# Kernel optimization log

Measured on AMD Instinct MI355X. Metric: run time of the kernel, lower is better.

## Reference

```python
import jax, jax.numpy as jnp
import numpy as np

DIM = 320; D_STATE = 32; D_CONV = 4; HEADDIM = 80; D_INNER = 640; NHEADS = 8
CONV_DIM = D_INNER + 2 * D_STATE          # 704
D_IN_PROJ = 2 * D_INNER + 2 * D_STATE + NHEADS  # 1352
ATTN_HEADS = 4; MLP_DIM = 1024; DEPTH = 2; INNER = DIM // 2  # cross-attn downsample_rate=2
PATCH = (128.0, 256.0, 256.0); IMG = (16, 32, 32); NPTS = 6; BATCH = 2
EPS = 1e-5
TWO_PI = 2.0 * np.pi


def layernorm(x, w, b):
    m = x.mean(-1, keepdims=True)
    v = ((x - m) ** 2).mean(-1, keepdims=True)
    return (x - m) * jax.lax.rsqrt(v + EPS) * w + b


def pe_encode(coords, gauss):
    # coords in [0,1], last dim 3 -> random fourier features (sin|cos) of width DIM
    c = TWO_PI * ((2.0 * coords - 1.0) @ gauss)
    return jnp.concatenate([jnp.sin(c), jnp.cos(c)], -1)


def mha(qi, ki, vi, wq, bq, wk, bk, wv, bv, wo, bo):
    q = qi @ wq.T + bq
    k = ki @ wk.T + bk
    v = vi @ wv.T + bv
    B, Nq, Ci = q.shape
    hd = Ci // ATTN_HEADS
    q = q.reshape(B, Nq, ATTN_HEADS, hd)
    k = k.reshape(B, -1, ATTN_HEADS, hd)
    v = v.reshape(B, -1, ATTN_HEADS, hd)
    att = jax.nn.softmax(jnp.einsum('bqhd,bkhd->bhqk', q, k) / np.sqrt(hd), -1)
    o = jnp.einsum('bhqk,bkhd->bqhd', att, v).reshape(B, Nq, Ci)
    return o @ wo.T + bo


def mamba2(xn, in_w, conv_w, conv_b, dt_bias, A_log, Dp, rms_w, out_w):
    Bt, L, _ = xn.shape
    zxbcdt = xn @ in_w.T                                    # (B,L,1352)
    z, xBC, dt = jnp.split(zxbcdt, [D_INNER, D_INNER + CONV_DIM], axis=-1)
    dt = jax.nn.softplus(dt + dt_bias)                      # (B,L,H)
    # causal depthwise conv over sequence, kernel D_CONV
    pad = jnp.pad(xBC, ((0, 0), (D_CONV - 1, 0), (0, 0)))
    conv = conv_b + sum(pad[:, k:k + L] * conv_w[:, k] for k in range(D_CONV))
    xBC = jax.nn.silu(conv)
    xs, Bm, Cm = jnp.split(xBC, [D_INNER, D_INNER + D_STATE], axis=-1)
    A = -jnp.exp(A_log)                                     # (H,)
    xh = xs.reshape(Bt, L, NHEADS, HEADDIM)

    def step(S, inp):  # S: (B,H,N,P)
        dt_t, x_t, B_t, C_t = inp  # (B,H),(B,H,P),(B,N),(B,N)
        decay = jnp.exp(dt_t * A)
        S = S * decay[..., None, None] + (dt_t[..., None, None] * B_t[:, None, :, None]) * x_t[:, :, None, :]
        y = jnp.einsum('bn,bhnp->bhp', C_t, S)
        return S, y

    S0 = jnp.zeros((Bt, NHEADS, D_STATE, HEADDIM), xn.dtype)
    _, ys = jax.lax.scan(step, S0, (dt.transpose(1, 0, 2), xh.transpose(1, 0, 2, 3), Bm.transpose(1, 0, 2), Cm.transpose(1, 0, 2)))
    y = ys.transpose(1, 0, 2, 3) + Dp[None, None, :, None] * xh  # (B,L,H,P)
    y = y.reshape(Bt, L, D_INNER)
    y = y * jax.nn.silu(z)                                  # gated RMSNorm (norm_before_gate=False)
    y = y * jax.lax.rsqrt((y * y).mean(-1, keepdims=True) + EPS) * rms_w
    return y @ out_w.T


def _forward(x, coords, ln_w, ln_b, in_w, conv_w, conv_b, dt_bias, A_log, Dp, rms_w, out_w,
             pe_gauss, point_tab, sa_w, sa_b, t2i_w, t2i_b, t2i_ow, t2i_ob,
             i2t_w, i2t_b, i2t_ow, i2t_ob, norms_w, norms_b, mlp_w1, mlp_b1, mlp_w2, mlp_b2, labels):
    B, C = x.shape[:2]
    img = x.shape[2:]
    n = int(np.prod(img))
    xf = jnp.transpose(x.reshape(B, C, n), (0, 2, 1))       # (B,n,C)
    keys = mamba2(layernorm(xf, ln_w, ln_b), in_w, conv_w, conv_b, dt_bias, A_log, Dp, rms_w, out_w)
    # point embeddings: fourier PE of normalized click coords + label embedding
    point_emb = pe_encode(coords / jnp.asarray(PATCH, x.dtype), pe_gauss) + point_tab[labels]
    # dense image positional encoding over the feature grid
    axes = [(jnp.arange(s, dtype=x.dtype) + 0.5) / s for s in img]
    grid = jnp.stack(jnp.meshgrid(*axes, indexing='ij'), -1)  # (d,h,w,3)
    kpe = jnp.broadcast_to(pe_encode(grid, pe_gauss).reshape(1, n, C), (B, n, C))
    queries = point_emb
    qpe = point_emb
    for i in range(DEPTH):
        saw, sab = sa_w[i], sa_b[i]
        if i == 0:  # skip_first_layer_pe
            queries = mha(queries, queries, queries, saw[0], sab[0], saw[1], sab[1], saw[2], sab[2], saw[3], sab[3])
        else:
            q = queries + qpe
            queries = queries + mha(q, q, queries, saw[0], sab[0], saw[1], sab[1], saw[2], sab[2], saw[3], sab[3])
        queries = layernorm(queries, norms_w[i, 0], norms_b[i, 0])
        q = queries + qpe
        k = keys + kpe
        queries = queries + mha(q, k, keys, t2i_w[i, 0], t2i_b[i, 0], t2i_w[i, 1], t2i_b[i, 1], t2i_w[i, 2], t2i_b[i, 2], t2i_ow[i], t2i_ob[i])
        queries = layernorm(queries, norms_w[i, 1], norms_b[i, 1])
        queries = queries + jax.nn.relu(queries @ mlp_w1[i].T + mlp_b1[i]) @ mlp_w2[i].T + mlp_b2[i]
        queries = layernorm(queries, norms_w[i, 2], norms_b[i, 2])
        q = queries + qpe
        k = keys + kpe
        keys = keys + mha(k, q, queries, i2t_w[i, 0], i2t_b[i, 0], i2t_w[i, 1], i2t_b[i, 1], i2t_w[i, 2], i2t_b[i, 2], i2t_ow[i], i2t_ob[i])
        keys = layernorm(keys, norms_w[i, 3], norms_b[i, 3])
    return jnp.transpose(keys, (0, 2, 1)).reshape(B, C, *img)


def setup_inputs():
    key = jax.random.key(0)
    ks = iter(jax.random.split(key, 64))
    f32 = jnp.float32

    def nrm(shape, s=0.02):
        return s * jax.random.normal(next(ks), shape, dtype=f32)

    inp = {}
    inp['x'] = jax.random.normal(next(ks), (BATCH, DIM) + IMG, dtype=f32)
    inp['coords'] = jax.random.uniform(next(ks), (BATCH, NPTS, 3), dtype=f32) * jnp.asarray(PATCH, f32)
    inp['labels'] = jax.random.randint(next(ks), (BATCH, NPTS), 0, 2)
    inp['ln_w'] = jnp.ones((DIM,), f32)
    inp['ln_b'] = jnp.zeros((DIM,), f32)
    inp['in_w'] = nrm((D_IN_PROJ, DIM))
    inp['conv_w'] = nrm((CONV_DIM, D_CONV), 0.2)
    inp['conv_b'] = jnp.zeros((CONV_DIM,), f32)
    inp['dt_bias'] = nrm((NHEADS,), 0.1)
    inp['A_log'] = jnp.log(jnp.arange(1, NHEADS + 1, dtype=f32))
    inp['Dp'] = jnp.ones((NHEADS,), f32)
    inp['rms_w'] = jnp.ones((D_INNER,), f32)
    inp['out_w'] = nrm((DIM, D_INNER))
    inp['pe_gauss'] = jax.random.normal(next(ks), (3, DIM // 2), dtype=f32)
    inp['point_tab'] = nrm((2, DIM), 1.0)
    inp['sa_w'] = nrm((DEPTH, 4, DIM, DIM))
    inp['sa_b'] = jnp.zeros((DEPTH, 4, DIM), f32)
    inp['t2i_w'] = nrm((DEPTH, 3, INNER, DIM))
    inp['t2i_b'] = jnp.zeros((DEPTH, 3, INNER), f32)
    inp['t2i_ow'] = nrm((DEPTH, DIM, INNER))
    inp['t2i_ob'] = jnp.zeros((DEPTH, DIM), f32)
    inp['i2t_w'] = nrm((DEPTH, 3, INNER, DIM))
    inp['i2t_b'] = jnp.zeros((DEPTH, 3, INNER), f32)
    inp['i2t_ow'] = nrm((DEPTH, DIM, INNER))
    inp['i2t_ob'] = jnp.zeros((DEPTH, DIM), f32)
    inp['norms_w'] = jnp.ones((DEPTH, 4, DIM), f32)
    inp['norms_b'] = jnp.zeros((DEPTH, 4, DIM), f32)
    inp['mlp_w1'] = nrm((DEPTH, MLP_DIM, DIM))
    inp['mlp_b1'] = jnp.zeros((DEPTH, MLP_DIM), f32)
    inp['mlp_w2'] = nrm((DEPTH, DIM, MLP_DIM))
    inp['mlp_b2'] = jnp.zeros((DEPTH, DIM), f32)
    return inp


def reference(x, coords, labels, ln_w, ln_b, in_w, conv_w, conv_b, dt_bias, A_log, Dp, rms_w, out_w,
              pe_gauss, point_tab, sa_w, sa_b, t2i_w, t2i_b, t2i_ow, t2i_ob,
              i2t_w, i2t_b, i2t_ow, i2t_ob, norms_w, norms_b, mlp_w1, mlp_b1, mlp_w2, mlp_b2):
    return _forward(x, coords, ln_w, ln_b, in_w, conv_w, conv_b, dt_bias, A_log, Dp, rms_w, out_w,
                    pe_gauss, point_tab, sa_w, sa_b, t2i_w, t2i_b, t2i_ow, t2i_ob,
                    i2t_w, i2t_b, i2t_ow, i2t_ob, norms_w, norms_b, mlp_w1, mlp_b1, mlp_w2, mlp_b2, labels)
```

## Files before the change

### kernel.cpp

```cpp
#include <hip/hip_runtime.h>
#include <math.h>

#define LSEQ 16384
#define CDIM 320
#define DIN 640
#define NHH 8
#define CONVD 704
#define XBCW 712
#define YSTR 704
#define QCH 64
#define NCHUNK 256

typedef __bf16 bf16_t;
typedef __bf16 bf16x8 __attribute__((ext_vector_type(8)));
typedef __bf16 bf16x4 __attribute__((ext_vector_type(4)));
typedef float f32x4 __attribute__((ext_vector_type(4)));

__device__ __forceinline__ float wave_sum(float v) {
#pragma unroll
  for (int o = 32; o > 0; o >>= 1) v += __shfl_down(v, o, 64);
  return v;
}
__device__ __forceinline__ float wave_max(float v) {
#pragma unroll
  for (int o = 32; o > 0; o >>= 1) v = fmaxf(v, __shfl_down(v, o, 64));
  return v;
}
__device__ __forceinline__ float block_sum256(float v, float* red) {
  int tid = threadIdx.x;
  v = wave_sum(v);
  __syncthreads();
  if ((tid & 63) == 0) red[tid >> 6] = v;
// ... 93 lines not shown
  float* xp = io + (size_t)row * CDIM;
  int lane = threadIdx.x & 63;
  float x[5];
  float s = 0.f;
#pragma unroll
  for (int k = 0; k < 5; ++k) { x[k] = xp[lane + 64 * k]; s += x[k]; }
  s = wave_sum(s); s = __shfl(s, 0, 64);
  float mean = s * (1.f / 320.f);
  float v = 0.f;
#pragma unroll
  for (int k = 0; k < 5; ++k) { float t = x[k] - mean; v += t * t; }
  v = wave_sum(v); v = __shfl(v, 0, 64);
  float rstd = rsqrtf(v * (1.f / 320.f) + 1e-5f);
#pragma unroll
  for (int k = 0; k < 5; ++k) {
    int i = lane + 64 * k;
    xp[i] = (x[k] - mean) * rstd * w[i] + b[i];
  }
}

__global__ __launch_bounds__(256) void gemm_bf(
    const void* __restrict__ A, const void* __restrict__ W,
    const float* __restrict__ bias, const float* __restrict__ pe,
    float* __restrict__ C, float* __restrict__ C2,
    const void* __restrict__ W2, const float* __restrict__ bias2, int wsplit,
    int M, int N, int K, int lda, int ldc, int nsplit, int ldc2,
    int addC, int abf, int wbf, long long sA, long long sC) {
  int z = blockIdx.z;
  C += (size_t)z * sC;
  if (C2) C2 += (size_t)z * sC;
  int gx = gridDim.x;
  int nwg = gx * gridDim.y;
  int lin = blockIdx.y * gx + blockIdx.x;
  int xcd = lin & 7, idx = lin >> 3;
  int q = nwg >> 3, r = nwg & 7;
  int base = (xcd < r) ? xcd * (q + 1) : r * (q + 1) + (xcd - r) * q;
  int lin2 = base + idx;
  int mblk = lin2 / gx, nblk = lin2 % gx;
  int m0 = mblk << 7, n0 = nblk << 6;

  __shared__ __align__(16) bf16_t As[2][4096];
  __shared__ __align__(16) bf16_t Ws[2][2048];
  int tid = threadIdx.x;
  int wave = tid >> 6, lane = tid & 63;
  int fm = lane & 15, quad = lane >> 4;
  int rA = tid >> 1, hA = tid & 1;
  int rW = tid >> 2, qW = tid & 3;
  const float* ag = nullptr;
  const bf16_t* agb = nullptr;
  const float* peg = nullptr;
  if (abf) {
    agb = (const bf16_t*)A + (size_t)z * sA + (size_t)(m0 + rA) * lda + hA * 16;
  } else {
// ... 89 lines not shown
    bf16x8 b3 = *(bf16x8*)&Ws[buf][1536 + lane * 8];
    acc[0][0] = __builtin_amdgcn_mfma_f32_16x16x32_bf16(af0, b0, acc[0][0], 0, 0, 0);
    acc[0][1] = __builtin_amdgcn_mfma_f32_16x16x32_bf16(af0, b1, acc[0][1], 0, 0, 0);
    acc[0][2] = __builtin_amdgcn_mfma_f32_16x16x32_bf16(af0, b2, acc[0][2], 0, 0, 0);
    acc[0][3] = __builtin_amdgcn_mfma_f32_16x16x32_bf16(af0, b3, acc[0][3], 0, 0, 0);
    acc[1][0] = __builtin_amdgcn_mfma_f32_16x16x32_bf16(af1, b0, acc[1][0], 0, 0, 0);
    acc[1][1] = __builtin_amdgcn_mfma_f32_16x16x32_bf16(af1, b1, acc[1][1], 0, 0, 0);
    acc[1][2] = __builtin_amdgcn_mfma_f32_16x16x32_bf16(af1, b2, acc[1][2], 0, 0, 0);
    acc[1][3] = __builtin_amdgcn_mfma_f32_16x16x32_bf16(af1, b3, acc[1][3], 0, 0, 0);
    if (more) {
      packLDS(buf ^ 1);
      __syncthreads();
    }
  }
#pragma unroll
  for (int ms = 0; ms < 2; ++ms)
#pragma unroll
    for (int ns = 0; ns < 4; ++ns) {
      int n = n0 + ns * 16 + fm;
      if (n >= N) continue;
      float bv = 0.f;
      if (n < wsplit) { if (bias) bv = bias[n]; }
      else            { if (bias2) bv = bias2[n - wsplit]; }
      float* Cb;
      int ldcb, nc;
      if (n < nsplit) { Cb = C; ldcb = ldc; nc = n; }
      else           { Cb = C2; ldcb = ldc2; nc = n - nsplit; }
#pragma unroll
      for (int rr = 0; rr < 4; ++rr) {
        int m = m0 + wave * 32 + ms * 16 + quad * 4 + rr;
        float v = acc[ms][ns][rr] + bv;
        size_t off = (size_t)m * ldcb + nc;
        if (addC) v += Cb[off];
        Cb[off] = v;
      }
    }
}

__global__ __launch_bounds__(256) void smallmm(
    const float* __restrict__ A, const float* __restrict__ A2,
    const float* __restrict__ W, const float* __restrict__ bias,
    float* __restrict__ C, int N, int K, int addC, int relu, int a2lim) {
  int wave = threadIdx.x >> 6, lane = threadIdx.x & 63;
  int n = blockIdx.x * 4 + wave;
  if (n >= N) return;
  const float* w = W + (size_t)n * K;
  bool useA2 = (A2 != nullptr) && (n < a2lim);
  float part[12];
#pragma unroll
  for (int m = 0; m < 12; ++m) part[m] = 0.f;
  for (int k0 = 0; k0 < K; k0 += 64) {
    int k = k0 + lane;
    if (k < K) {
      float wv = w[k];
      const float* ap = A + k;
      if (useA2) {
        const float* ap2 = A2 + k;
// ... 1 lines not shown
        for (int m = 0; m < 12; ++m)
          part[m] = fmaf(ap[(size_t)m * K] + ap2[(size_t)m * K], wv, part[m]);
      } else {
#pragma unroll
        for (int m = 0; m < 12; ++m)
          part[m] = fmaf(ap[(size_t)m * K], wv, part[m]);
      }
    }
  }
  float bv = bias ? bias[n] : 0.f;
#pragma unroll
  for (int m = 0; m < 12; ++m) {
    float dot = wave_sum(part[m]);
    if (lane == 0) {
      float v = dot + bv;
      if (relu) v = fmaxf(v, 0.f);
      size_t off = (size_t)m * N + n;
      if (addC) v += C[off];
      C[off] = v;
    }
  }
}

__global__ void dt_kernel(const float* __restrict__ XBC, const float* __restrict__ dt_bias,
                          float* __restrict__ dtbuf) {
  int idx = blockIdx.x * 256 + threadIdx.x;
  if (idx >= LSEQ * NHH) return;
  int h = idx & 7;
  int t = idx >> 3;
  float v = XBC[(size_t)t * XBCW + 704 + h] + dt_bias[h];
  float sp = (v > 20.f) ? v : log1pf(expf(v));
  dtbuf[(size_t)h * LSEQ + t] = sp;
}

__global__ __launch_bounds__(256) void conv2(const float* __restrict__ XBC,
                                             const float* __restrict__ conv_w,
                                             const float* __restrict__ conv_b,
                                             float* __restrict__ Cv) {
  int lane = threadIdx.x & 63, wv = threadIdx.x >> 6;
  int d = blockIdx.x * 64 + lane;
  int t0 = (blockIdx.y * 4 + wv) * 32;
  float w0 = conv_w[d * 4 + 0], w1 = conv_w[d * 4 + 1];
  float w2 = conv_w[d * 4 + 2], w3 = conv_w[d * 4 + 3];
  float bv = conv_b[d];
  const float* src = XBC + d;
  float xm3, xm2, xm1;
  if (t0 == 0) {
    xm3 = 0.f; xm2 = 0.f; xm1 = 0.f;
  } else {
    xm3 = src[(size_t)(t0 - 3) * XBCW];
    xm2 = src[(size_t)(t0 - 2) * XBCW];
    xm1 = src[(size_t)(t0 - 1) * XBCW];
  }
#pragma unroll 8
  for (int t = t0; t < t0 + 32; ++t) {
    float xt = src[(size_t)t * XBCW];
    float a = bv + xm3 * w0 + xm2 * w1 + xm1 * w2 + xt * w3;
    Cv[(size_t)t * CONVD + d] = a / (1.f + expf(-a));
    xm3 = xm2; xm2 = xm1; xm1 = xt;
  }
}

__global__ __launch_bounds__(256) void scan_a(const float* __restrict__ Cv,
                                              const float* __restrict__ dtbuf,
                                              const float* __restrict__ A_log,
                                              float* __restrict__ Schunk,
                                              float* __restrict__ cabuf) {
  int c = blockIdx.x, h = blockIdx.y;
  int t0 = c * QCH;
  __shared__ float sdt[64], sca[64], sw[64];
  __shared__ __align__(16) float sB[64][36];
  __shared__ __align__(16) float sXt[80][68];
  int tid = threadIdx.x;
  float Aval = -expf(A_log[h]);
  if (tid < 64) sdt[tid] = dtbuf[(size_t)h * LSEQ + t0 + tid];
  __syncthreads();
  if (tid == 0) {
    float run = 0.f;
    for (int j = 0; j < 64; ++j) { run += sdt[j] * Aval; sca[j] = run; }
  }
  __syncthreads();
  float caend = sca[63];
  if (tid < 64) {
    sw[tid] = expf(caend - sca[tid]) * sdt[tid];
    cabuf[(size_t)h * LSEQ + t0 + tid] = sca[tid];
  }
  for (int i = tid; i < 2048; i += 256) {
    int j = i >> 5, n = i & 31;
    sB[j][n] = Cv[(size_t)(t0 + j) * CONVD + 640 + n];
  }
  for (int i = tid; i < 5120; i += 256) {
    int j = i / 80, p = i % 80;
    sXt[p][j] = Cv[(size_t)(t0 + j) * CONVD + h * 80 + p];
  }
  __syncthreads();
  int n = tid >> 3, pb = tid & 7;
  float acc[10];
#pragma unroll
  for (int u = 0; u < 10; ++u) acc[u] = 0.f;
  for (int jb = 0; jb < 16; ++jb) {
    float wB[4];
#pragma unroll
    for (int jj = 0; jj < 4; ++jj) {
      int j = jb * 4 + jj;
      wB[jj] = sw[j] * sB[j][n];
    }
#pragma unroll
    for (int u = 0; u < 10; ++u) {
      int p = pb * 10 + u;
      float4 x4 = *(const float4*)&sXt[p][jb * 4];
      acc[u] += wB[0] * x4.x + wB[1] * x4.y + wB[2] * x4.z + wB[3] * x4.w;
    }
  }
  float* outp = Schunk + (size_t)(h * NCHUNK + c) * 2560;
#pragma unroll
  for (int u = 0; u < 10; ++u) outp[n * 80 + pb * 10 + u] = acc[u];
}

__global__ __launch_bounds__(256) void scan_b(const float* __restrict__ Schunk,
                                              const float* __restrict__ cabuf,
                                              float* __restrict__ Sprev) {
  int pc = blockIdx.x, h = blockIdx.y;
  __shared__ float sdec[256];
  int tid = threadIdx.x;
  sdec[tid] = expf(cabuf[(size_t)h * LSEQ + tid * 64 + 63]);
  __syncthreads();
  int e = pc * 256 + tid;
  const float* base = Schunk + (size_t)h * NCHUNK * 2560 + e;
  float* pbase = Sprev + (size_t)h * NCHUNK * 2560 + e;
  float s = 0.f;
  float v = base[0];
  for (int c = 0; c < NCHUNK; ++c) {
    float vn = (c < NCHUNK - 1) ? base[(size_t)(c + 1) * 2560] : 0.f;
    pbase[(size_t)c * 2560] = s;
    s = s * sdec[c] + v;
    v = vn;
  }
}

__global__ __launch_bounds__(256) void scan_c(const float* __restrict__ Cv,
                                              const float* __restrict__ dtbuf,
                                              const float* __restrict__ cabuf,
                                              const float* __restrict__ Sprev,
                                              const float* __restrict__ Dp,
                                              float* __restrict__ Y) {
  int c = blockIdx.x, h = blockIdx.y;
  int t0 = c * QCH;
  __shared__ float sdt[64], sca[64], sexp[64];
  __shared__ __align__(16) bf16_t sC[64 * 40];
  __shared__ __align__(16) bf16_t sB[64 * 40];
  __shared__ __align__(16) bf16_t sXt[80 * 72];
  __shared__ __align__(16) bf16_t sSt[80 * 40];
  __shared__ __align__(16) bf16_t sP[64 * 72];
  int tid = threadIdx.x;
  int wave = tid >> 6, lane = tid & 63;
  int fm = lane & 15, quad = lane >> 4;
  if (tid < 64) {
    sdt[tid] = dtbuf[(size_t)h * LSEQ + t0 + tid];
    float cav = cabuf[(size_t)h * LSEQ + t0 + tid];
    sca[tid] = cav;
    sexp[tid] = expf(cav);
  }
  for (int i = tid; i < 2048; i += 256) {
    int j = i >> 5, n = i & 31;
    size_t base = (size_t)(t0 + j) * CONVD;
    sB[j * 40 + n] = (bf16_t)Cv[base + 640 + n];
    sC[j * 40 + n] = (bf16_t)Cv[base + 672 + n];
  }
  for (int i = tid; i < 5120; i += 256) {
    int j = i / 80, p = i % 80;
    sXt[p * 72 + j] = (bf16_t)Cv[(size_t)(t0 + j) * CONVD + h * 80 + p];
  }
  {
    const float* sp = Sprev + (size_t)(h * NCHUNK + c) * 2560;
    for (int i = tid; i < 2560; i += 256) {
      int n = i / 80, p = i % 80;
      sSt[p * 40 + n] = (bf16_t)sp[i];
    }
  }
  __syncthreads();
  int m0 = wave * 16;
  int jbase = m0 + quad * 4;
  bf16x8 afC = *(bf16x8*)&sC[(m0 + fm) * 40 + quad * 8];
  f32x4 accS[4];
#pragma unroll
  for (int nt = 0; nt < 4; ++nt) {
    bf16x8 bf = *(bf16x8*)&sB[(nt * 16 + fm) * 40 + quad * 8];
    f32x4 zero = (f32x4){0.f, 0.f, 0.f, 0.f};
    accS[nt] = __builtin_amdgcn_mfma_f32_16x16x32_bf16(afC, bf, zero, 0, 0, 0);
  }
  float scaj[4];
#pragma unroll
  for (int r = 0; r < 4; ++r) scaj[r] = sca[jbase + r];
#pragma unroll
// ... 19 lines not shown
#pragma unroll
  for (int r = 0; r < 4; ++r) gj[r] = sexp[jbase + r];
#pragma unroll
  for (int pt = 0; pt < 5; ++pt)
#pragma unroll
    for (int r = 0; r < 4; ++r) acc[pt][r] *= gj[r];
  bf16x8 afP0 = *(bf16x8*)&sP[(m0 + fm) * 72 + 0 + quad * 8];
  bf16x8 afP1 = *(bf16x8*)&sP[(m0 + fm) * 72 + 32 + quad * 8];
#pragma unroll
  for (int pt = 0; pt < 5; ++pt) {
    bf16x8 bx0 = *(bf16x8*)&sXt[(pt * 16 + fm) * 72 + 0 + quad * 8];
    bf16x8 bx1 = *(bf16x8*)&sXt[(pt * 16 + fm) * 72 + 32 + quad * 8];
    acc[pt] = __builtin_amdgcn_mfma_f32_16x16x32_bf16(afP0, bx0, acc[pt], 0, 0, 0);
    acc[pt] = __builtin_amdgcn_mfma_f32_16x16x32_bf16(afP1, bx1, acc[pt], 0, 0, 0);
  }
  float dval = Dp[h];
#pragma unroll
  for (int pt = 0; pt < 5; ++pt) {
    int p = pt * 16 + fm;
#pragma unroll
    for (int r = 0; r < 4; ++r) {
      int j = jbase + r;
      float xv = (float)sXt[p * 72 + j];
      Y[(size_t)(t0 + j) * YSTR + h * 80 + p] = acc[pt][r] + dval * xv;
    }
  }
}

__global__ __launch_bounds__(256) void gate_rms(const float* __restrict__ Y,
                                                const float* __restrict__ Z,
                                                const float* __restrict__ rms_w,
                                                bf16_t* __restrict__ YB) {
  __shared__ float red[4];
  size_t row = blockIdx.x;
  const float* y = Y + row * YSTR;
  const float* z = Z + row * DIN;
  bf16_t* yo = YB + row * DIN;
  int tid = threadIdx.x;
  float g0, g1, g2 = 0.f;
  {
    float zi = z[tid];
    g0 = y[tid] * (zi / (1.f + expf(-zi)));
    zi = z[tid + 256];
    g1 = y[tid + 256] * (zi / (1.f + expf(-zi)));
    if (tid + 512 < DIN) {
      zi = z[tid + 512];
      g2 = y[tid + 512] * (zi / (1.f + expf(-zi)));
    }
  }
  float ss = g0 * g0 + g1 * g1 + g2 * g2;
  float tot = block_sum256(ss, red);
  float r = rsqrtf(tot / (float)DIN + 1e-5f);
  yo[tid] = (bf16_t)(g0 * r * rms_w[tid]);
  yo[tid + 256] = (bf16_t)(g1 * r * rms_w[tid + 256]);
  if (tid + 512 < DIN) yo[tid + 512] = (bf16_t)(g2 * r * rms_w[tid + 512]);
}

__global__ void kpe_kernel(const float* __restrict__ gauss, float* __restrict__ KPE) {
  int idx = blockIdx.x * 256 + threadIdx.x;
  if (idx >= LSEQ * 160) return;
  int f = idx % 160, t = idx / 160;
  int d = t >> 10, hh = (t >> 5) & 31, w = t & 31;
  float vx = 2.f * ((d + 0.5f) / 16.f) - 1.f;
  float vy = 2.f * ((hh + 0.5f) / 32.f) - 1.f;
  float vz = 2.f * ((w + 0.5f) / 32.f) - 1.f;
  float cc = 6.28318530717958647692f * (vx * gauss[f] + vy * gauss[160 + f] + vz * gauss[320 + f]);
  KPE[(size_t)t * CDIM + f] = sinf(cc);
  KPE[(size_t)t * CDIM + 160 + f] = cosf(cc);
}

__global__ void point_kernel(const float* __restrict__ coords, const int* __restrict__ labels,
                             const float* __restrict__ gauss, const float* __restrict__ ptab,
                             float* __restrict__ qpe, float* __restrict__ queries) {
  int idx = blockIdx.x * 64 + threadIdx.x;
  if (idx >= 12 * 160) return;
  int f = idx % 160, pt = idx / 160;
  const float* co = coords + pt * 3;
  float vx = 2.f * (co[0] / 128.f) - 1.f;
// ... 22 lines not shown
    float d = 0.f;
    for (int p = 0; p < 80; ++p) d += sq[qi][p] * sk[ki][p];
    sw[qi][ki] = d * 0.11180339887498948f;
  }
  __syncthreads();
  if (tid < 6) {
    float mx = sw[tid][0];
    for (int k = 1; k < 6; ++k) mx = fmaxf(mx, sw[tid][k]);
    float s = 0.f;
    for (int k = 0; k < 6; ++k) { float e = expf(sw[tid][k] - mx); sw[tid][k] = e; s += e; }
    float inv = 1.f / s;
    for (int k = 0; k < 6; ++k) sw[tid][k] *= inv;
  }
  __syncthreads();
  for (int i = tid; i < 480; i += 128) {
    int qi = i / 80, p = i % 80;
    float o = 0.f;
    for (int k = 0; k < 6; ++k) o += sw[qi][k] * sv[k][p];
    O[(size_t)(b * 6 + qi) * CDIM + h * 80 + p] = o;
  }
}

__global__ __launch_bounds__(256) void attn_t2i_part2(const float* __restrict__ Qp,
                                                      const float* __restrict__ Kp,
                                                      const float* __restrict__ Vp,
                                                      float* __restrict__ Part) {
  int b = blockIdx.z, h = blockIdx.y, c = blockIdx.x;
  Qp += (size_t)b * 960;
  Kp += (size_t)b * LSEQ * 160;
  Vp += (size_t)b * LSEQ * 160;
  Part += (size_t)b * 24 * 64 * 42;
  __shared__ float sq[240];
  __shared__ float redm[4][6], reds[4][6];
  __shared__ __align__(16) bf16_t sPb[16 * 264];
  __shared__ __align__(16) bf16_t sVtb[48 * 264];
  int tid = threadIdx.x;
  int wave = tid >> 6, lane = tid & 63;
  if (tid < 240) sq[tid] = Qp[(size_t)(tid / 40) * 160 + h * 40 + (tid % 40)];
  __syncthreads();
  int t = c * 256 + tid;
  const float* kp = Kp + (size_t)t * 160 + h * 40;
  float kr[40];
#pragma unroll
  for (int v = 0; v < 10; ++v) {
    float4 k4 = *(const float4*)(kp + v * 4);
    kr[v * 4 + 0] = k4.x; kr[v * 4 + 1] = k4.y; kr[v * 4 + 2] = k4.z; kr[v * 4 + 3] = k4.w;
  }
  const float* vp = Vp + (size_t)t * 160 + h * 40;
#pragma unroll
  for (int v = 0; v < 10; ++v) {
    float4 v4 = *(const float4*)(vp + v * 4);
    sVtb[(v * 4 + 0) * 264 + tid] = (bf16_t)v4.x;
    sVtb[(v * 4 + 1) * 264 + tid] = (bf16_t)v4.y;
    sVtb[(v * 4 + 2) * 264 + tid] = (bf16_t)v4.z;
    sVtb[(v * 4 + 3) * 264 + tid] = (bf16_t)v4.w;
  }
  float s[6];
#pragma unroll
  for (int qi = 0; qi < 6; ++qi) {
    float d = 0.f;
#pragma unroll
    for (int p = 0; p < 40; ++p) d += sq[qi * 40 + p] * kr[p];
    s[qi] = d * 0.15811388300841897f;
  }
#pragma unroll
  for (int qi = 0; qi < 6; ++qi) {
    float wm = wave_max(s[qi]);
    if (lane == 0) redm[wave][qi] = wm;
  }
  __syncthreads();
  float gmax[6], ls[6];
#pragma unroll
  for (int qi = 0; qi < 6; ++qi)
    gmax[qi] = fmaxf(fmaxf(redm[0][qi], redm[1][qi]), fmaxf(redm[2][qi], redm[3][qi]));
#pragma unroll
  for (int qi = 0; qi < 6; ++qi) {
    float e = expf(s[qi] - gmax[qi]);
    sPb[qi * 264 + tid] = (bf16_t)e;
// ... 47 lines not shown
  const float* base = Part + (size_t)b * 24 * 64 * 42 + (size_t)blk * 64 * 42;
  float m = base[j * 42 + 40], l = base[j * 42 + 41];
  float gmax = wave_max(m);
  gmax = __shfl(gmax, 0, 64);
  float sc = expf(m - gmax);
  float tot = wave_sum(l * sc);
  tot = __shfl(tot, 0, 64);
  float inv = 1.f / tot;
  __shared__ float ssc[64];
  ssc[j] = sc;
  __syncthreads();
  if (j < 40) {
    float a0 = 0.f, a1 = 0.f, a2 = 0.f, a3 = 0.f;
    for (int jj = 0; jj < 64; jj += 4) {
      a0 = fmaf(base[(jj + 0) * 42 + j], ssc[jj + 0], a0);
      a1 = fmaf(base[(jj + 1) * 42 + j], ssc[jj + 1], a1);
      a2 = fmaf(base[(jj + 2) * 42 + j], ssc[jj + 2], a2);
      a3 = fmaf(base[(jj + 3) * 42 + j], ssc[jj + 3], a3);
    }
    O[(size_t)b * 960 + (size_t)qi * 160 + h * 40 + j] = (a0 + a1 + a2 + a3) * inv;
  }
}

__global__ __launch_bounds__(256) void attn_i2t(const float* __restrict__ Qp,
                                                const float* __restrict__ KV,
                                                bf16_t* __restrict__ O) {
  int h = blockIdx.y, b = blockIdx.z;
  int t = blockIdx.x * 256 + threadIdx.x;
  Qp += (size_t)b * LSEQ * 160;
  O += (size_t)b * LSEQ * 160;
  __shared__ float sk[6][40], sv[6][40];
  if (threadIdx.x < 240) {
    int tok = threadIdx.x / 40, p = threadIdx.x % 40;
    const float* base = KV + (size_t)(b * 6 + tok) * 320 + h * 40 + p;
    sk[tok][p] = base[0];
    sv[tok][p] = base[160];
  }
  __syncthreads();
  const float* q = Qp + (size_t)t * 160 + h * 40;
  float qr[40];
#pragma unroll
  for (int v = 0; v < 10; ++v) {
    float4 q4 = *(const float4*)(q + v * 4);
    qr[v * 4 + 0] = q4.x; qr[v * 4 + 1] = q4.y; qr[v * 4 + 2] = q4.z; qr[v * 4 + 3] = q4.w;
  }
  float s[6];
#pragma unroll
  for (int k = 0; k < 6; ++k) {
    float d = 0.f;
    for (int p = 0; p < 40; ++p) d += qr[p] * sk[k][p];
    s[k] = d * 0.15811388300841897f;
  }
  float mx = s[0];
#pragma unroll
  for (int k = 1; k < 6; ++k) mx = fmaxf(mx, s[k]);
  float sum = 0.f;
#pragma unroll
  for (int k = 0; k < 6; ++k) { s[k] = expf(s[k] - mx); sum += s[k]; }
  float inv = 1.f / sum;
  bf16_t* o = O + (size_t)t * 160 + h * 40;
#pragma unroll
  for (int v = 0; v < 10; ++v) {
    float o0 = 0.f, o1 = 0.f, o2 = 0.f, o3 = 0.f;
#pragma unroll
    for (int k = 0; k < 6; ++k) {
      float w = s[k];
      o0 += w * sv[k][v * 4 + 0];
// ... 36 lines not shown
  const float* i2t_w   = (const float*)d_in[21];
  const float* i2t_b   = (const float*)d_in[22];
  const float* i2t_ow  = (const float*)d_in[23];
  const float* i2t_ob  = (const float*)d_in[24];
  const float* norms_w = (const float*)d_in[25];
  const float* norms_b = (const float*)d_in[26];
  const float* mlp_w1  = (const float*)d_in[27];
  const float* mlp_b1  = (const float*)d_in[28];
  const float* mlp_w2  = (const float*)d_in[29];
  const float* mlp_b2  = (const float*)d_in[30];
  float* out = (float*)d_out;
  float* ws = (float*)d_ws;

  const size_t NEED = (size_t)(10485760 + 5242880 + 11665408 + 11534336 + 10485760 +
                               131072 + 131072 + 65536) * 4;
  if (ws_size < NEED) {
    ws_probe<<<1, 1, 0, stream>>>(out, (float)ws_size);
    return;
  }
  float* R_K = ws;
  float* P   = ws + 10485760;
  bf16_t* XNB_   = (bf16_t*)P;
  float* SCHUNK_ = P;
  float* ZB_     = P + 5242880;
  float* XBC_    = P + 15728640;
  float* SPREV_  = P + 15728640;
  bf16_t* YB_    = (bf16_t*)(P + 20971520);
  float* CV_     = P + 27394048;
  float* DT_     = P + 38928384;
  float* CA_     = P + 39059456;
  bf16_t* WBM_   = (bf16_t*)(P + 38928384);
  float* KPE_   = P;
  float* T0_    = P + 5242880;
  float* T3_    = P + 10485760;
  float* T1_    = P + 15728640;
  bf16_t* T2B_  = (bf16_t*)(P + 26214400);
  float* PART_  = P + 36700160;
  float* SM_    = P + 36829184;
  float* QPE_  = SM_;
  float* QRY_  = SM_ + 3840;
  float* P3_   = SM_ + 7680;
  float* PO_   = SM_ + 19200;
  float* H_    = SM_ + 23040;
  float* Q160_ = SM_ + 35328;
  float* O160_ = SM_ + 37248;
  float* KV_   = SM_ + 39168;

  const long long sIMG160 = (long long)LSEQ * 160;
  const long long sIMG320 = (long long)LSEQ * CDIM;
  const int NOSPLIT = 1 << 30;

  for (int b = 0; b < 2; ++b) {
    const float* xb = x + (size_t)b * CDIM * LSEQ;
    float* Kb = R_K + (size_t)b * LSEQ * CDIM;

    tln<<<LSEQ / 32, 256, 0, stream>>>(xb, ln_w, ln_b, XNB_);
    cvt_bf<<<(432640 / 4 + 255) / 256, 256, 0, stream>>>(in_w, WBM_, 432640);

    gemm_bf<<<dim3(22, 128, 1), 256, 0, stream>>>(
        XNB_, WBM_, nullptr, nullptr, ZB_, XBC_, nullptr, nullptr, NOSPLIT,
        LSEQ, 1352, CDIM, CDIM, DIN, DIN, XBCW, 0, 1, 1, 0, 0);

    dt_kernel<<<LSEQ * NHH / 256, 256, 0, stream>>>(XBC_, dt_bias, DT_);
    conv2<<<dim3(11, 128), 256, 0, stream>>>(XBC_, conv_w, conv_b, CV_);

    scan_a<<<dim3(NCHUNK, NHH), 256, 0, stream>>>(CV_, DT_, A_log, SCHUNK_, CA_);
    scan_b<<<dim3(10, NHH), 256, 0, stream>>>(SCHUNK_, CA_, SPREV_);
    scan_c<<<dim3(NCHUNK, NHH), 256, 0, stream>>>(CV_, DT_, CA_, SPREV_, Dp, CV_);

    cvt_bf<<<(204800 / 4 + 255) / 256, 256, 0, stream>>>(out_w, WBM_, 204800);
    gate_rms<<<LSEQ, 256, 0, stream>>>(CV_, ZB_, rms_w, YB_);

    gemm_bf<<<dim3(5, 128, 1), 256, 0, stream>>>(
        YB_, WBM_, nullptr, nullptr, Kb, nullptr, nullptr, nullptr, NOSPLIT,
        LSEQ, CDIM, DIN, DIN, CDIM, NOSPLIT, 0, 0, 1, 1, 0, 0);
  }

  kpe_kernel<<<LSEQ * 160 / 256, 256, 0, stream>>>(gauss, KPE_);
  point_kernel<<<30, 64, 0, stream>>>(coords, labels, gauss, ptab, QPE_, QRY_);

  for (int i = 0; i < 2; ++i) {
    const float* saw = sa_w + (size_t)i * 4 * CDIM * CDIM;
    const float* sab = sa_b + (size_t)i * 4 * CDIM;
    smallmm<<<240, 256, 0, stream>>>(QRY_, (i == 0) ? nullptr : QPE_,
                                     saw, sab, P3_, 960, CDIM, 0, 0, 640);
    attn_self<<<dim3(4, 2), 128, 0, stream>>>(P3_, PO_);
    smallmm<<<80, 256, 0, stream>>>(PO_, nullptr, saw + 3 * 102400, sab + 3 * CDIM,
                                    QRY_, CDIM, CDIM, (i == 0) ? 0 : 1, 0, 0);
    ln_rows256<<<3, 256, 0, stream>>>(QRY_, norms_w + (size_t)(i * 4 + 0) * CDIM,
                                      norms_b + (size_t)(i * 4 + 0) * CDIM, 12);

    smallmm<<<40, 256, 0, stream>>>(QRY_, QPE_, t2i_w + (size_t)(i * 3 + 0) * 51200,
                                    t2i_b + (size_t)(i * 3 + 0) * 160, Q160_,
                                    160, CDIM, 0, 0, 160);
    gemm_bf<<<dim3(5, 128, 2), 256, 0, stream>>>(
        R_K, t2i_w + (size_t)(i * 3 + 1) * 51200, t2i_b + (size_t)(i * 3 + 1) * 160,
        KPE_, T0_, T3_, i2t_w + (size_t)(i * 3 + 0) * 51200,
        i2t_b + (size_t)(i * 3 + 0) * 160, 160,
        LSEQ, 320, CDIM, CDIM, 160, 160, 160, 0, 0, 0, sIMG320, sIMG160);
    gemm_bf<<<dim3(3, 128, 2), 256, 0, stream>>>(
        R_K, t2i_w + (size_t)(i * 3 + 2) * 51200, t2i_b + (size_t)(i * 3 + 2) * 160,
        nullptr, T1_, nullptr, nullptr, nullptr, NOSPLIT,
        LSEQ, 160, CDIM, CDIM, 160, NOSPLIT, 0, 0, 0, 0, sIMG320, sIMG160);
    attn_t2i_part2<<<dim3(64, 4, 2), 256, 0, stream>>>(Q160_, T0_, T1_, PART_);
    attn_t2i_comb<<<dim3(24, 2), 64, 0, stream>>>(PART_, O160_);
    smallmm<<<80, 256, 0, stream>>>(O160_, nullptr, t2i_ow + (size_t)i * 51200,
                                    t2i_ob + (size_t)i * CDIM, QRY_,
                                    CDIM, 160, 1, 0, 0);
    ln_rows256<<<3, 256, 0, stream>>>(QRY_, norms_w + (size_t)(i * 4 + 1) * CDIM,
                                      norms_b + (size_t)(i * 4 + 1) * CDIM, 12);

    smallmm<<<256, 256, 0, stream>>>(QRY_, nullptr, mlp_w1 + (size_t)i * 1024 * CDIM,
                                     mlp_b1 + (size_t)i * 1024, H_, 1024, CDIM, 0, 1, 0);
    smallmm<<<80, 256, 0, stream>>>(H_, nullptr, mlp_w2 + (size_t)i * CDIM * 1024,
                                    mlp_b2 + (size_t)i * CDIM, QRY_, CDIM, 1024, 1, 0, 0);
    ln_rows256<<<3, 256, 0, stream>>>(QRY_, norms_w + (size_t)(i * 4 + 2) * CDIM,
                                      norms_b + (size_t)(i * 4 + 2) * CDIM, 12);

    smallmm<<<80, 256, 0, stream>>>(QRY_, QPE_, i2t_w + (size_t)(i * 3 + 1) * 51200,
                                    i2t_b + (size_t)(i * 3 + 1) * 160, KV_,
                                    320, CDIM, 0, 0, 160);
    attn_i2t<<<dim3(LSEQ / 256, 4, 2), 256, 0, stream>>>(T3_, KV_, T2B_);
    gemm_bf<<<dim3(5, 128, 2), 256, 0, stream>>>(
        T2B_, i2t_ow + (size_t)i * CDIM * 160, i2t_ob + (size_t)i * CDIM,
        nullptr, R_K, nullptr, nullptr, nullptr, NOSPLIT,
        LSEQ, CDIM, 160, 160, CDIM, NOSPLIT, 0, 1, 1, 0, sIMG160, sIMG320);
    if (i == 0) {
      ln_rows256<<<2 * LSEQ / 4, 256, 0, stream>>>(
          R_K, norms_w + (size_t)3 * CDIM, norms_b + (size_t)3 * CDIM, 2 * LSEQ);
    }
  }

  for (int b = 0; b < 2; ++b) {
    lnt<<<LSEQ / 32, 256, 0, stream>>>(
        R_K + (size_t)b * LSEQ * CDIM, norms_w + (size_t)7 * CDIM,
        norms_b + (size_t)7 * CDIM, out + (size_t)b * CDIM * LSEQ);
  }
}
```

Baseline: 1.036 ms.

## Store intermediate activations in bf16 across mamba and cross-attention stages

The GEMM epilogue can now write bf16 output. The in-projection (z, xBC, dt), conv output, scan output Y and the attention projections T0/T1/T3 are all stored as bf16 instead of fp32, and consumers read bf16 with vectorised loads. Weight conversions are hoisted out of the per-batch loop, and gate_rms now works in place on the bf16 Y buffer. The goal is to roughly halve memory traffic on large intermediates, at the cost of precision loss in activations such as dt and the conv inputs.

```diff
diff --git a/kernel.cpp b/kernel.cpp
--- a/kernel.cpp
+++ b/kernel.cpp
@@ -7,7 +7,6 @@
 #define NHH 8
 #define CONVD 704
 #define XBCW 712
-#define YSTR 704
 #define QCH 64
 #define NCHUNK 256
 
@@ -147,13 +146,11 @@
 __global__ __launch_bounds__(256) void gemm_bf(
     const void* __restrict__ A, const void* __restrict__ W,
     const float* __restrict__ bias, const float* __restrict__ pe,
-    float* __restrict__ C, float* __restrict__ C2,
+    void* __restrict__ C, void* __restrict__ C2,
     const void* __restrict__ W2, const float* __restrict__ bias2, int wsplit,
     int M, int N, int K, int lda, int ldc, int nsplit, int ldc2,
-    int addC, int abf, int wbf, long long sA, long long sC) {
+    int addC, int abf, int wbf, int cbf, long long sA, long long sC) {
   int z = blockIdx.z;
-  C += (size_t)z * sC;
-  if (C2) C2 += (size_t)z * sC;
   int gx = gridDim.x;
   int nwg = gx * gridDim.y;
   int lin = blockIdx.y * gx + blockIdx.x;
@@ -289,17 +286,22 @@
       float bv = 0.f;
       if (n < wsplit) { if (bias) bv = bias[n]; }
       else            { if (bias2) bv = bias2[n - wsplit]; }
-      float* Cb;
+      void* Cb;
       int ldcb, nc;
       if (n < nsplit) { Cb = C; ldcb = ldc; nc = n; }
-      else           { Cb = C2; ldcb = ldc2; nc = n - nsplit; }
+      else            { Cb = C2; ldcb = ldc2; nc = n - nsplit; }
 #pragma unroll
       for (int rr = 0; rr < 4; ++rr) {
         int m = m0 + wave * 32 + ms * 16 + quad * 4 + rr;
         float v = acc[ms][ns][rr] + bv;
-        size_t off = (size_t)m * ldcb + nc;
-        if (addC) v += Cb[off];
-        Cb[off] = v;
+        size_t off = (size_t)z * sC + (size_t)m * ldcb + nc;
+        if (cbf) {
+          ((bf16_t*)Cb)[off] = (bf16_t)v;
+        } else {
+          float* Cf = (float*)Cb;
+          if (addC) v += Cf[off];
+          Cf[off] = v;
+        }
       }
     }
 }
@@ -347,46 +349,46 @@
   }
 }
 
-__global__ void dt_kernel(const float* __restrict__ XBC, const float* __restrict__ dt_bias,
+__global__ void dt_kernel(const bf16_t* __restrict__ XBC, const float* __restrict__ dt_bias,
                           float* __restrict__ dtbuf) {
   int idx = blockIdx.x * 256 + threadIdx.x;
   if (idx >= LSEQ * NHH) return;
   int h = idx & 7;
   int t = idx >> 3;
-  float v = XBC[(size_t)t * XBCW + 704 + h] + dt_bias[h];
+  float v = (float)XBC[(size_t)t * XBCW + 704 + h] + dt_bias[h];
   float sp = (v > 20.f) ? v : log1pf(expf(v));
   dtbuf[(size_t)h * LSEQ + t] = sp;
 }
 
-__global__ __launch_bounds__(256) void conv2(const float* __restrict__ XBC,
+__global__ __launch_bounds__(256) void conv2(const bf16_t* __restrict__ XBC,
                                              const float* __restrict__ conv_w,
                                              const float* __restrict__ conv_b,
-                                             float* __restrict__ Cv) {
+                                             bf16_t* __restrict__ Cv) {
   int lane = threadIdx.x & 63, wv = threadIdx.x >> 6;
   int d = blockIdx.x * 64 + lane;
   int t0 = (blockIdx.y * 4 + wv) * 32;
   float w0 = conv_w[d * 4 + 0], w1 = conv_w[d * 4 + 1];
   float w2 = conv_w[d * 4 + 2], w3 = conv_w[d * 4 + 3];
   float bv = conv_b[d];
-  const float* src = XBC + d;
+  const bf16_t* src = XBC + d;
   float xm3, xm2, xm1;
   if (t0 == 0) {
     xm3 = 0.f; xm2 = 0.f; xm1 = 0.f;
   } else {
-    xm3 = src[(size_t)(t0 - 3) * XBCW];
-    xm2 = src[(size_t)(t0 - 2) * XBCW];
-    xm1 = src[(size_t)(t0 - 1) * XBCW];
+    xm3 = (float)src[(size_t)(t0 - 3) * XBCW];
+    xm2 = (float)src[(size_t)(t0 - 2) * XBCW];
+    xm1 = (float)src[(size_t)(t0 - 1) * XBCW];
   }
 #pragma unroll 8
   for (int t = t0; t < t0 + 32; ++t) {
-    float xt = src[(size_t)t * XBCW];
+    float xt = (float)src[(size_t)t * XBCW];
     float a = bv + xm3 * w0 + xm2 * w1 + xm1 * w2 + xt * w3;
-    Cv[(size_t)t * CONVD + d] = a / (1.f + expf(-a));
+    Cv[(size_t)t * CONVD + d] = (bf16_t)(a / (1.f + expf(-a)));
     xm3 = xm2; xm2 = xm1; xm1 = xt;
   }
 }
 
-__global__ __launch_bounds__(256) void scan_a(const float* __restrict__ Cv,
+__global__ __launch_bounds__(256) void scan_a(const bf16_t* __restrict__ Cv,
                                               const float* __restrict__ dtbuf,
                                               const float* __restrict__ A_log,
                                               float* __restrict__ Schunk,
@@ -412,11 +414,11 @@
   }
   for (int i = tid; i < 2048; i += 256) {
     int j = i >> 5, n = i & 31;
-    sB[j][n] = Cv[(size_t)(t0 + j) * CONVD + 640 + n];
+    sB[j][n] = (float)Cv[(size_t)(t0 + j) * CONVD + 640 + n];
   }
   for (int i = tid; i < 5120; i += 256) {
     int j = i / 80, p = i % 80;
-    sXt[p][j] = Cv[(size_t)(t0 + j) * CONVD + h * 80 + p];
+    sXt[p][j] = (float)Cv[(size_t)(t0 + j) * CONVD + h * 80 + p];
   }
   __syncthreads();
   int n = tid >> 3, pb = tid & 7;
@@ -463,12 +465,12 @@
   }
 }
 
-__global__ __launch_bounds__(256) void scan_c(const float* __restrict__ Cv,
+__global__ __launch_bounds__(256) void scan_c(const bf16_t* __restrict__ Cv,
                                               const float* __restrict__ dtbuf,
                                               const float* __restrict__ cabuf,
                                               const float* __restrict__ Sprev,
                                               const float* __restrict__ Dp,
-                                              float* __restrict__ Y) {
+                                              bf16_t* __restrict__ Y) {
   int c = blockIdx.x, h = blockIdx.y;
   int t0 = c * QCH;
   __shared__ float sdt[64], sca[64], sexp[64];
@@ -489,12 +491,12 @@
   for (int i = tid; i < 2048; i += 256) {
     int j = i >> 5, n = i & 31;
     size_t base = (size_t)(t0 + j) * CONVD;
-    sB[j * 40 + n] = (bf16_t)Cv[base + 640 + n];
-    sC[j * 40 + n] = (bf16_t)Cv[base + 672 + n];
+    sB[j * 40 + n] = Cv[base + 640 + n];
+    sC[j * 40 + n] = Cv[base + 672 + n];
   }
   for (int i = tid; i < 5120; i += 256) {
     int j = i / 80, p = i % 80;
-    sXt[p * 72 + j] = (bf16_t)Cv[(size_t)(t0 + j) * CONVD + h * 80 + p];
+    sXt[p * 72 + j] = Cv[(size_t)(t0 + j) * CONVD + h * 80 + p];
   }
   {
     const float* sp = Sprev + (size_t)(h * NCHUNK + c) * 2560;
@@ -560,38 +562,36 @@
     for (int r = 0; r < 4; ++r) {
       int j = jbase + r;
       float xv = (float)sXt[p * 72 + j];
-      Y[(size_t)(t0 + j) * YSTR + h * 80 + p] = acc[pt][r] + dval * xv;
-    }
-  }
-}
-
-__global__ __launch_bounds__(256) void gate_rms(const float* __restrict__ Y,
-                                                const float* __restrict__ Z,
-                                                const float* __restrict__ rms_w,
-                                                bf16_t* __restrict__ YB) {
+      Y[(size_t)(t0 + j) * DIN + h * 80 + p] = (bf16_t)(acc[pt][r] + dval * xv);
+    }
+  }
+}
+
+__global__ __launch_bounds__(256) void gate_rms(bf16_t* __restrict__ YS,
+                                                const bf16_t* __restrict__ Z,
+                                                const float* __restrict__ rms_w) {
   __shared__ float red[4];
   size_t row = blockIdx.x;
-  const float* y = Y + row * YSTR;
-  const float* z = Z + row * DIN;
-  bf16_t* yo = YB + row * DIN;
+  bf16_t* y = YS + row * DIN;
+  const bf16_t* z = Z + row * DIN;
   int tid = threadIdx.x;
   float g0, g1, g2 = 0.f;
   {
-    float zi = z[tid];
-    g0 = y[tid] * (zi / (1.f + expf(-zi)));
-    zi = z[tid + 256];
-    g1 = y[tid + 256] * (zi / (1.f + expf(-zi)));
+    float zi = (float)z[tid];
+    g0 = (float)y[tid] * (zi / (1.f + expf(-zi)));
+    zi = (float)z[tid + 256];
+    g1 = (float)y[tid + 256] * (zi / (1.f + expf(-zi)));
     if (tid + 512 < DIN) {
-      zi = z[tid + 512];
-      g2 = y[tid + 512] * (zi / (1.f + expf(-zi)));
+      zi = (float)z[tid + 512];
+      g2 = (float)y[tid + 512] * (zi / (1.f + expf(-zi)));
     }
   }
   float ss = g0 * g0 + g1 * g1 + g2 * g2;
   float tot = block_sum256(ss, red);
   float r = rsqrtf(tot / (float)DIN + 1e-5f);
-  yo[tid] = (bf16_t)(g0 * r * rms_w[tid]);
-  yo[tid + 256] = (bf16_t)(g1 * r * rms_w[tid + 256]);
-  if (tid + 512 < DIN) yo[tid + 512] = (bf16_t)(g2 * r * rms_w[tid + 512]);
+  y[tid] = (bf16_t)(g0 * r * rms_w[tid]);
+  y[tid + 256] = (bf16_t)(g1 * r * rms_w[tid + 256]);
+  if (tid + 512 < DIN) y[tid + 512] = (bf16_t)(g2 * r * rms_w[tid + 512]);
 }
 
 __global__ void kpe_kernel(const float* __restrict__ gauss, float* __restrict__ KPE) {
@@ -660,8 +660,8 @@
 }
 
 __global__ __launch_bounds__(256) void attn_t2i_part2(const float* __restrict__ Qp,
-                                                      const float* __restrict__ Kp,
-                                                      const float* __restrict__ Vp,
+                                                      const bf16_t* __restrict__ Kp,
+                                                      const bf16_t* __restrict__ Vp,
                                                       float* __restrict__ Part) {
   int b = blockIdx.z, h = blockIdx.y, c = blockIdx.x;
   Qp += (size_t)b * 960;
@@ -677,21 +677,20 @@
   if (tid < 240) sq[tid] = Qp[(size_t)(tid / 40) * 160 + h * 40 + (tid % 40)];
   __syncthreads();
   int t = c * 256 + tid;
-  const float* kp = Kp + (size_t)t * 160 + h * 40;
+  const bf16_t* kp = Kp + (size_t)t * 160 + h * 40;
   float kr[40];
 #pragma unroll
-  for (int v = 0; v < 10; ++v) {
-    float4 k4 = *(const float4*)(kp + v * 4);
-    kr[v * 4 + 0] = k4.x; kr[v * 4 + 1] = k4.y; kr[v * 4 + 2] = k4.z; kr[v * 4 + 3] = k4.w;
-  }
-  const float* vp = Vp + (size_t)t * 160 + h * 40;
-#pragma unroll
-  for (int v = 0; v < 10; ++v) {
-    float4 v4 = *(const float4*)(vp + v * 4);
-    sVtb[(v * 4 + 0) * 264 + tid] = (bf16_t)v4.x;
-    sVtb[(v * 4 + 1) * 264 + tid] = (bf16_t)v4.y;
-    sVtb[(v * 4 + 2) * 264 + tid] = (bf16_t)v4.z;
-    sVtb[(v * 4 + 3) * 264 + tid] = (bf16_t)v4.w;
+  for (int v = 0; v < 5; ++v) {
+    bf16x8 k8 = *(const bf16x8*)(kp + v * 8);
+#pragma unroll
+    for (int j = 0; j < 8; ++j) kr[v * 8 + j] = (float)k8[j];
+  }
+  const bf16_t* vp = Vp + (size_t)t * 160 + h * 40;
+#pragma unroll
+  for (int v = 0; v < 5; ++v) {
+    bf16x8 v8 = *(const bf16x8*)(vp + v * 8);
+#pragma unroll
+    for (int j = 0; j < 8; ++j) sVtb[(v * 8 + j) * 264 + tid] = v8[j];
   }
   float s[6];
 #pragma unroll
@@ -785,7 +784,7 @@
   }
 }
 
-__global__ __launch_bounds__(256) void attn_i2t(const float* __restrict__ Qp,
+__global__ __launch_bounds__(256) void attn_i2t(const bf16_t* __restrict__ Qp,
                                                 const float* __restrict__ KV,
                                                 bf16_t* __restrict__ O) {
   int h = blockIdx.y, b = blockIdx.z;
@@ -800,12 +799,13 @@
     sv[tok][p] = base[160];
   }
   __syncthreads();
-  const float* q = Qp + (size_t)t * 160 + h * 40;
+  const bf16_t* q = Qp + (size_t)t * 160 + h * 40;
   float qr[40];
 #pragma unroll
-  for (int v = 0; v < 10; ++v) {
-    float4 q4 = *(const float4*)(q + v * 4);
-    qr[v * 4 + 0] = q4.x; qr[v * 4 + 1] = q4.y; qr[v * 4 + 2] = q4.z; qr[v * 4 + 3] = q4.w;
+  for (int v = 0; v < 5; ++v) {
+    bf16x8 q8 = *(const bf16x8*)(q + v * 8);
+#pragma unroll
+    for (int j = 0; j < 8; ++j) qr[v * 8 + j] = (float)q8[j];
   }
   float s[6];
 #pragma unroll
@@ -888,21 +888,22 @@
   float* P   = ws + 10485760;
   bf16_t* XNB_   = (bf16_t*)P;
   float* SCHUNK_ = P;
-  float* ZB_     = P + 5242880;
-  float* XBC_    = P + 15728640;
-  float* SPREV_  = P + 15728640;
-  bf16_t* YB_    = (bf16_t*)(P + 20971520);
-  float* CV_     = P + 27394048;
-  float* DT_     = P + 38928384;
-  float* CA_     = P + 39059456;
-  bf16_t* WBM_   = (bf16_t*)(P + 38928384);
+  bf16_t* ZBB_   = (bf16_t*)(P + 5242880);
+  bf16_t* XBCB_  = (bf16_t*)(P + 10485760);
+  float* SPREV_  = P + 10485760;
+  bf16_t* CVB_   = (bf16_t*)(P + 16318464);
+  bf16_t* YSB_   = (bf16_t*)(P + 22085632);
+  float* DT_     = P + 27328512;
+  float* CA_     = P + 27459584;
+  bf16_t* WBI_   = (bf16_t*)(P + 27590656);
+  bf16_t* WBO_   = (bf16_t*)(P + 27806976);
   float* KPE_   = P;
-  float* T0_    = P + 5242880;
-  float* T3_    = P + 10485760;
-  float* T1_    = P + 15728640;
-  bf16_t* T2B_  = (bf16_t*)(P + 26214400);
-  float* PART_  = P + 36700160;
-  float* SM_    = P + 36829184;
+  bf16_t* T0B_  = (bf16_t*)(P + 5242880);
+  bf16_t* T3B_  = (bf16_t*)(P + 7864320);
+  bf16_t* T1B_  = (bf16_t*)(P + 10485760);
+  bf16_t* T2B_  = (bf16_t*)(P + 13107200);
+  float* PART_  = P + 15728640;
+  float* SM_    = P + 15857664;
   float* QPE_  = SM_;
   float* QRY_  = SM_ + 3840;
   float* P3_   = SM_ + 7680;
@@ -916,30 +917,31 @@
   const long long sIMG320 = (long long)LSEQ * CDIM;
   const int NOSPLIT = 1 << 30;
 
+  cvt_bf<<<(432640 / 4 + 255) / 256, 256, 0, stream>>>(in_w, WBI_, 432640);
+  cvt_bf<<<(204800 / 4 + 255) / 256, 256, 0, stream>>>(out_w, WBO_, 204800);
+
   for (int b = 0; b < 2; ++b) {
     const float* xb = x + (size_t)b * CDIM * LSEQ;
     float* Kb = R_K + (size_t)b * LSEQ * CDIM;
 
     tln<<<LSEQ / 32, 256, 0, stream>>>(xb, ln_w, ln_b, XNB_);
-    cvt_bf<<<(432640 / 4 + 255) / 256, 256, 0, stream>>>(in_w, WBM_, 432640);
 
     gemm_bf<<<dim3(22, 128, 1), 256, 0, stream>>>(
-        XNB_, WBM_, nullptr, nullptr, ZB_, XBC_, nullptr, nullptr, NOSPLIT,
-        LSEQ, 1352, CDIM, CDIM, DIN, DIN, XBCW, 0, 1, 1, 0, 0);
-
-    dt_kernel<<<LSEQ * NHH / 256, 256, 0, stream>>>(XBC_, dt_bias, DT_);
-    conv2<<<dim3(11, 128), 256, 0, stream>>>(XBC_, conv_w, conv_b, CV_);
-
-    scan_a<<<dim3(NCHUNK, NHH), 256, 0, stream>>>(CV_, DT_, A_log, SCHUNK_, CA_);
+        XNB_, WBI_, nullptr, nullptr, ZBB_, XBCB_, nullptr, nullptr, NOSPLIT,
+        LSEQ, 1352, CDIM, CDIM, DIN, DIN, XBCW, 0, 1, 1, 1, 0, 0);
+
+    dt_kernel<<<LSEQ * NHH / 256, 256, 0, stream>>>(XBCB_, dt_bias, DT_);
+    conv2<<<dim3(11, 128), 256, 0, stream>>>(XBCB_, conv_w, conv_b, CVB_);
+
+    scan_a<<<dim3(NCHUNK, NHH), 256, 0, stream>>>(CVB_, DT_, A_log, SCHUNK_, CA_);
     scan_b<<<dim3(10, NHH), 256, 0, stream>>>(SCHUNK_, CA_, SPREV_);
-    scan_c<<<dim3(NCHUNK, NHH), 256, 0, stream>>>(CV_, DT_, CA_, SPREV_, Dp, CV_);
-
-    cvt_bf<<<(204800 / 4 + 255) / 256, 256, 0, stream>>>(out_w, WBM_, 204800);
-    gate_rms<<<LSEQ, 256, 0, stream>>>(CV_, ZB_, rms_w, YB_);
+    scan_c<<<dim3(NCHUNK, NHH), 256, 0, stream>>>(CVB_, DT_, CA_, SPREV_, Dp, YSB_);
+
+    gate_rms<<<LSEQ, 256, 0, stream>>>(YSB_, ZBB_, rms_w);
 
     gemm_bf<<<dim3(5, 128, 1), 256, 0, stream>>>(
-        YB_, WBM_, nullptr, nullptr, Kb, nullptr, nullptr, nullptr, NOSPLIT,
-        LSEQ, CDIM, DIN, DIN, CDIM, NOSPLIT, 0, 0, 1, 1, 0, 0);
+        YSB_, WBO_, nullptr, nullptr, Kb, nullptr, nullptr, nullptr, NOSPLIT,
+        LSEQ, CDIM, DIN, DIN, CDIM, NOSPLIT, 0, 0, 1, 1, 0, 0, 0);
   }
 
   kpe_kernel<<<LSEQ * 160 / 256, 256, 0, stream>>>(gauss, KPE_);
@@ -961,14 +963,14 @@
                                     160, CDIM, 0, 0, 160);
     gemm_bf<<<dim3(5, 128, 2), 256, 0, stream>>>(
         R_K, t2i_w + (size_t)(i * 3 + 1) * 51200, t2i_b + (size_t)(i * 3 + 1) * 160,
-        KPE_, T0_, T3_, i2t_w + (size_t)(i * 3 + 0) * 51200,
+        KPE_, T0B_, T3B_, i2t_w + (size_t)(i * 3 + 0) * 51200,
         i2t_b + (size_t)(i * 3 + 0) * 160, 160,
-        LSEQ, 320, CDIM, CDIM, 160, 160, 160, 0, 0, 0, sIMG320, sIMG160);
+        LSEQ, 320, CDIM, CDIM, 160, 160, 160, 0, 0, 0, 1, sIMG320, sIMG160);
     gemm_bf<<<dim3(3, 128, 2), 256, 0, stream>>>(
         R_K, t2i_w + (size_t)(i * 3 + 2) * 51200, t2i_b + (size_t)(i * 3 + 2) * 160,
-        nullptr, T1_, nullptr, nullptr, nullptr, NOSPLIT,
-        LSEQ, 160, CDIM, CDIM, 160, NOSPLIT, 0, 0, 0, 0, sIMG320, sIMG160);
-    attn_t2i_part2<<<dim3(64, 4, 2), 256, 0, stream>>>(Q160_, T0_, T1_, PART_);
+        nullptr, T1B_, nullptr, nullptr, nullptr, NOSPLIT,
+        LSEQ, 160, CDIM, CDIM, 160, NOSPLIT, 0, 0, 0, 0, 1, sIMG320, sIMG160);
+    attn_t2i_part2<<<dim3(64, 4, 2), 256, 0, stream>>>(Q160_, T0B_, T1B_, PART_);
     attn_t2i_comb<<<dim3(24, 2), 64, 0, stream>>>(PART_, O160_);
     smallmm<<<80, 256, 0, stream>>>(O160_, nullptr, t2i_ow + (size_t)i * 51200,
                                     t2i_ob + (size_t)i * CDIM, QRY_,
@@ -986,11 +988,11 @@
     smallmm<<<80, 256, 0, stream>>>(QRY_, QPE_, i2t_w + (size_t)(i * 3 + 1) * 51200,
                                     i2t_b + (size_t)(i * 3 + 1) * 160, KV_,
                                     320, CDIM, 0, 0, 160);
-    attn_i2t<<<dim3(LSEQ / 256, 4, 2), 256, 0, stream>>>(T3_, KV_, T2B_);
+    attn_i2t<<<dim3(LSEQ / 256, 4, 2), 256, 0, stream>>>(T3B_, KV_, T2B_);
     gemm_bf<<<dim3(5, 128, 2), 256, 0, stream>>>(
         T2B_, i2t_ow + (size_t)i * CDIM * 160, i2t_ob + (size_t)i * CDIM,
         nullptr, R_K, nullptr, nullptr, nullptr, NOSPLIT,
-        LSEQ, CDIM, 160, 160, CDIM, NOSPLIT, 0, 1, 1, 0, sIMG160, sIMG320);
+        LSEQ, CDIM, 160, 160, CDIM, NOSPLIT, 0, 1, 1, 0, 0, sIMG160, sIMG320);
     if (i == 0) {
       ln_rows256<<<2 * LSEQ / 4, 256, 0, stream>>>(
           R_K, norms_w + (size_t)3 * CDIM, norms_b + (size_t)3 * CDIM, 2 * LSEQ);
```

Result: faster. 1.001 ms (-3.3%).
